# Kernel tuning notes

Hardware: AMD Instinct MI355X
Metric: run time of the kernel (lower is better)

## Reference

```python
import jax, jax.numpy as jnp
import numpy as np

CONFIDENCE = 0.1
EPS = 1e-3  # keras BatchNormalization default epsilon
B, H, W, C = 4, 64, 64, 256


def setup_inputs() -> dict:
    key = jax.random.key(0)
    ks = jax.random.split(key, 6)
    return {
        "x": jax.random.normal(ks[0], (B, H, W, C), jnp.float32),
        "ca_gamma": jnp.ones((C,), jnp.float32),
        "ca_beta": jnp.zeros((C,), jnp.float32),
        "ca_mean": jnp.zeros((C,), jnp.float32),
        "ca_var": jnp.ones((C,), jnp.float32),
        "wq": jax.random.normal(ks[1], (C, C), jnp.float32) * 0.05,
        "wk": jax.random.normal(ks[2], (C, C), jnp.float32) * 0.05,
        "wv": jax.random.normal(ks[3], (C, C), jnp.float32) * 0.05,
        "wp": jax.random.normal(ks[4], (C, C), jnp.float32) * 0.05,
        "bn_gamma": jnp.ones((C,), jnp.float32),
        "bn_beta": jnp.zeros((C,), jnp.float32),
        "bn_mean": jnp.zeros((C,), jnp.float32),
        "bn_var": jnp.ones((C,), jnp.float32),
        "w_qkv": jax.random.normal(ks[5], (C, 3), jnp.float32) * 0.05,
    }


def _bn(x, g, b, m, v):
    # keras BatchNormalization, inference mode
    return (x - m) * jax.lax.rsqrt(v + EPS) * g + b


def reference(x, ca_gamma, ca_beta, ca_mean, ca_var, wq, wk, wv, wp,
              bn_gamma, bn_beta, bn_mean, bn_var, w_qkv):
    b, h, w, c = x.shape
    # ---- ChannelAttention (TRACER Channel_Tracer; dropout = identity at inference) ----
    gap = x.mean(axis=(1, 2))                         # [B, C] global average pool
    gn = _bn(gap, ca_gamma, ca_beta, ca_mean, ca_var)  # [B, C]
    q = gn @ wq                                        # 1x1 conv on 1x1 map == matmul
    k = gn @ wk
    v = gn @ wv
    logits = q[:, :, None] * k[:, None, :]             # [B, C, C], head_dim = 1
    score = jax.nn.softmax(logits, axis=-1)
    att = jnp.einsum('bij,bj->bi', score, v)           # [B, C]
    cmask = jax.nn.sigmoid(att @ wp)                   # [B, C] channel mask (alpha)
    ca_out = x * cmask[:, None, None, :] + x           # residual channel re-weighting
    # ---- UnionAttention spatial part ----
    co = _bn(ca_out, bn_gamma, bn_beta, bn_mean, bn_var)
    thr = jnp.percentile(cmask, CONFIDENCE * 100.0, axis=-1,
                         keepdims=True, method='linear')  # [B, 1]
    pmask = jnp.where(cmask > thr, cmask, 0.0)          # percentile masking
    co = co * pmask[:, None, None, :]
    qkv = jnp.einsum('bhwc,cf->bhwf', co, w_qkv)        # [B, H, W, 3] fused q/k/v 1x1 conv
    n = h * w
    qs = qkv[..., 0].reshape(b, n)                      # [B, N], head_dim = 1
    ks_ = qkv[..., 1].reshape(b, n)
    vs = qkv[..., 2].reshape(b, n)
    sl = qs[:, :, None] * ks_[:, None, :]               # [B, N, N] scores (outer product)
    sw = jax.nn.softmax(sl, axis=-1)
    sa = jnp.einsum('bij,bj->bi', sw, vs)               # [B, N]
    return qkv[..., 2:3] + sa.reshape(b, h, w, 1)       # v + attention, [B, H, W, 1]
```

## Files before the change

kernel.cpp:

```cpp
#include <hip/hip_runtime.h>

#define EPS 1e-3f

#define OFF_PGAP   0
#define OFF_A      65536
#define OFF_BIAS   66560
#define OFF_QS     66576
#define OFF_KS     82960
#define OFF_VS     99344
#define OFF_PART   115728

__global__ __launch_bounds__(256) void k_gap(const float* __restrict__ x,
                                             float* __restrict__ pgap) {
    int blk = blockIdx.x;
    int t = threadIdx.x;
    const float* xp = x + (size_t)blk * (64 * 256) + t;
    float s = 0.f;
    #pragma unroll 16
    for (int p = 0; p < 64; ++p) s += xp[(size_t)p * 256];
    pgap[blk * 256 + t] = s;
}

__global__ __launch_bounds__(512) void k_mid(
    const float* __restrict__ pgap,
    const float* __restrict__ cag, const float* __restrict__ cab,
    const float* __restrict__ cam, const float* __restrict__ cav,
    const float* __restrict__ wq, const float* __restrict__ wk,
    const float* __restrict__ wv, const float* __restrict__ wp,
    const float* __restrict__ bng, const float* __restrict__ bnb,
    const float* __restrict__ bnm, const float* __restrict__ bnv,
    const float* __restrict__ wqkv,
    float* __restrict__ Aout, float* __restrict__ biasOut)
{
    __shared__ float gn[256];
    __shared__ float sq[256], sk[256], sv[256], att[256], cm[256], Bc[256];
    __shared__ float red[6144];
    __shared__ float swqkv[768];
    __shared__ float t25, t26, thr;

    int b = blockIdx.x;
    int t = threadIdx.x;
    int cg = t & 63;
    int rg = t >> 6;
    int c4 = cg * 4;

    if (t < 384) {
        swqkv[t] = wqkv[t];
        if (t < 384) swqkv[t + 384] = wqkv[t + 384];
    }

    {
        const float* pg = pgap + (size_t)(b * 64 + rg * 8) * 256 + c4;
        float4 s = make_float4(0.f, 0.f, 0.f, 0.f);
        #pragma unroll
        for (int u = 0; u < 8; ++u) {
            float4 v = *(const float4*)(pg + (size_t)u * 256);
            s.x += v.x; s.y += v.y; s.z += v.z; s.w += v.w;
        }
        *(float4*)(red + rg * 256 + c4) = s;
    }
    __syncthreads();
    if (t < 256) {
        float g = 0.f;
        #pragma unroll
        for (int r = 0; r < 8; ++r) g += red[r * 256 + t];
        g *= (1.0f / 4096.0f);
        float sc = cag[t] * rsqrtf(cav[t] + EPS);
        gn[t] = g * sc + (cab[t] - cam[t] * sc);
    }
    __syncthreads();

    {
        int rbase = rg * 32;
        float4 aq = make_float4(0.f, 0.f, 0.f, 0.f);
        float4 ak = aq, av = aq;
        const float* wqp = wq + (size_t)rbase * 256 + c4;
        const float* wkp = wk + (size_t)rbase * 256 + c4;
        const float* wvp = wv + (size_t)rbase * 256 + c4;
        #pragma unroll 8
        for (int i = 0; i < 32; ++i) {
            float g = gn[rbase + i];
            float4 w = *(const float4*)(wqp + (size_t)i * 256);
            aq.x = fmaf(g, w.x, aq.x); aq.y = fmaf(g, w.y, aq.y);
            aq.z = fmaf(g, w.z, aq.z); aq.w = fmaf(g, w.w, aq.w);
        }
        #pragma unroll 8
        for (int i = 0; i < 32; ++i) {
            float g = gn[rbase + i];
            float4 w = *(const float4*)(wkp + (size_t)i * 256);
            ak.x = fmaf(g, w.x, ak.x); ak.y = fmaf(g, w.y, ak.y);
            ak.z = fmaf(g, w.z, ak.z); ak.w = fmaf(g, w.w, ak.w);
        }
        #pragma unroll 8
        for (int i = 0; i < 32; ++i) {
            float g = gn[rbase + i];
            float4 w = *(const float4*)(wvp + (size_t)i * 256);
            av.x = fmaf(g, w.x, av.x); av.y = fmaf(g, w.y, av.y);
            av.z = fmaf(g, w.z, av.z); av.w = fmaf(g, w.w, av.w);
        }
        *(float4*)(red + (0 * 8 + rg) * 256 + c4) = aq;
        *(float4*)(red + (1 * 8 + rg) * 256 + c4) = ak;
        *(float4*)(red + (2 * 8 + rg) * 256 + c4) = av;
    }
    __syncthreads();
    {
        int m = t >> 8, c = t & 255;
        float s = 0.f;
        #pragma unroll
        for (int r = 0; r < 8; ++r) s += red[(m * 8 + r) * 256 + c];
        if (m == 0) sq[c] = s; else sk[c] = s;
        if (t < 256) {
            float s2 = 0.f;
            #pragma unroll
            for (int r = 0; r < 8; ++r) s2 += red[(2 * 8 + r) * 256 + t];
            sv[t] = s2;
        }
    }
    __syncthreads();

    {
        int h = t >> 8, c = t & 255;
        float a = sq[c];
        int jb = h * 128;
        float mx = -1e30f;
        #pragma unroll 8
        for (int j = 0; j < 128; ++j) mx = fmaxf(mx, a * sk[jb + j]);
        float den = 0.f, num = 0.f;
        #pragma unroll 4
        for (int j = 0; j < 128; ++j) {
            float e = __expf(a * sk[jb + j] - mx);
            den += e; num = fmaf(e, sv[jb + j], num);
        }
        red[h * 256 + c] = mx;
        red[512 + h * 256 + c] = den;
        red[1024 + h * 256 + c] = num;
    }
    __syncthreads();
    if (t < 256) {
        float m0 = red[t], m1 = red[256 + t];
        float M = fmaxf(m0, m1);
        float s0 = __expf(m0 - M), s1 = __expf(m1 - M);
        float den = red[512 + t] * s0 + red[768 + t] * s1;
        float num = red[1024 + t] * s0 + red[1280 + t] * s1;
        att[t] = num / den;
    }
    __syncthreads();

    {
        int rbase = rg * 32;
        float4 ac = make_float4(0.f, 0.f, 0.f, 0.f);
        const float* wpp = wp + (size_t)rbase * 256 + c4;
        #pragma unroll 8
        for (int i = 0; i < 32; ++i) {
            float g = att[rbase + i];
            float4 w = *(const float4*)(wpp + (size_t)i * 256);
            ac.x = fmaf(g, w.x, ac.x); ac.y = fmaf(g, w.y, ac.y);
            ac.z = fmaf(g, w.z, ac.z); ac.w = fmaf(g, w.w, ac.w);
        }
        *(float4*)(red + rg * 256 + c4) = ac;
    }
    __syncthreads();
    if (t < 256) {
        float ac = 0.f;
        #pragma unroll
        for (int r = 0; r < 8; ++r) ac += red[r * 256 + t];
        cm[t] = 1.0f / (1.0f + __expf(-ac));
    }
    __syncthreads();

    if (t < 256) {
        float my = cm[t];
        int rank = 0;
        for (int j = 0; j < 256; ++j) {
            float o = cm[j];
            rank += (o < my) ? 1 : ((o == my && j < t) ? 1 : 0);
        }
        if (rank == 25) t25 = my;
        if (rank == 26) t26 = my;
    }
    __syncthreads();
    if (t == 0) thr = t25 + 0.5f * (t26 - t25);
    __syncthreads();

    if (t < 256) {
        float s2 = bng[t] * rsqrtf(bnv[t] + EPS);
        float o2 = bnb[t] - bnm[t] * s2;
        float cc = cm[t];
        float pm = (cc > thr) ? cc : 0.f;
        Aout[b * 256 + t] = (1.f + cc) * s2 * pm;
        Bc[t] = o2 * pm;
    }
    __syncthreads();
    if (t < 3) {
        float s3 = 0.f;
        for (int ch = 0; ch < 256; ++ch) s3 = fmaf(Bc[ch], swqkv[ch * 3 + t], s3);
        biasOut[b * 3 + t] = s3;
    }
}

__global__ __launch_bounds__(256) void k_qkv(
    const float* __restrict__ x, const float* __restrict__ A,
    const float* __restrict__ wqkv, const float* __restrict__ bias,
    float* __restrict__ qs, float* __restrict__ ks, float* __restrict__ vs)
{
    int lane = threadIdx.x & 63;
    int wid = (blockIdx.x * 256 + threadIdx.x) >> 6;
    float4 wA = *(const float4*)(wqkv + 12 * lane);
    float4 wB = *(const float4*)(wqkv + 12 * lane + 4);
    float4 wC = *(const float4*)(wqkv + 12 * lane + 8);
    float w00 = wA.x, w01 = wA.y, w02 = wA.z;
    float w10 = wA.w, w11 = wB.x, w12 = wB.y;
    float w20 = wB.z, w21 = wB.w, w22 = wC.x;
    float w30 = wC.y, w31 = wC.z, w32 = wC.w;
    #pragma unroll
    for (int b = 0; b < 4; ++b) {
        int pix = b * 4096 + wid;
        float4 xv = *(const float4*)(x + (size_t)pix * 256 + 4 * lane);
        float4 A4 = *(const float4*)(A + b * 256 + 4 * lane);
        float t0 = xv.x * A4.x, t1 = xv.y * A4.y;
        float t2 = xv.z * A4.z, t3 = xv.w * A4.w;
        float q = t0 * w00 + t1 * w10 + t2 * w20 + t3 * w30;
        float k = t0 * w01 + t1 * w11 + t2 * w21 + t3 * w31;
        float v = t0 * w02 + t1 * w12 + t2 * w22 + t3 * w32;
        #pragma unroll
        for (int m = 1; m < 64; m <<= 1) {
            q += __shfl_xor(q, m, 64);
            k += __shfl_xor(k, m, 64);
            v += __shfl_xor(v, m, 64);
        }
        if (lane == 0) {
            qs[pix] = q + bias[b * 3 + 0];
            ks[pix] = k + bias[b * 3 + 1];
            vs[pix] = v + bias[b * 3 + 2];
        }
    }
}

__global__ __launch_bounds__(256) void k_attn(
    const float* __restrict__ qs, const float* __restrict__ ks, const float* __restrict__ vs,
    float* __restrict__ part)
{
    __shared__ float4 skv4[256];
    __shared__ float wmx[4], wmn[4];
    int blk = blockIdx.x;
    int b = blk >> 7, rem = blk & 127;
    int ic = rem >> 3, jc = rem & 7;
    int t = threadIdx.x;
    int base = b * 4096, jb = jc * 512;
    float2 kp = ((const float2*)(ks + base + jb))[t];
    float2 vp = ((const float2*)(vs + base + jb))[t];
    skv4[t] = make_float4(kp.x, vp.x, kp.y, vp.y);
    float mx = fmaxf(kp.x, kp.y);
    float mn = fminf(kp.x, kp.y);
    #pragma unroll
    for (int m2 = 1; m2 < 64; m2 <<= 1) {
        mx = fmaxf(mx, __shfl_xor(mx, m2, 64));
        mn = fminf(mn, __shfl_xor(mn, m2, 64));
    }
    if ((t & 63) == 0) { wmx[t >> 6] = mx; wmn[t >> 6] = mn; }
    __syncthreads();
    mx = fmaxf(fmaxf(wmx[0], wmx[1]), fmaxf(wmx[2], wmx[3]));
    mn = fminf(fminf(wmn[0], wmn[1]), fminf(wmn[2], wmn[3]));

    int i = ic * 256 + t;
    float a = qs[base + i];
    float m = (a >= 0.f) ? a * mx : a * mn;
    float den0 = 0.f, num0 = 0.f, den1 = 0.f, num1 = 0.f;
    #pragma unroll 4
    for (int j2 = 0; j2 < 256; ++j2) {
        float4 kv = skv4[j2];
        float e0 = __expf(a * kv.x - m);
        float e1 = __expf(a * kv.z - m);
        den0 += e0; num0 = fmaf(e0, kv.y, num0);
        den1 += e1; num1 = fmaf(e1, kv.w, num1);
    }
    ((float4*)part)[(size_t)(base + i) * 8 + jc] =
        make_float4(den0 + den1, num0 + num1, m, 0.f);
}

__global__ __launch_bounds__(256) void k_out(
    const float* __restrict__ part, const float* __restrict__ vs,
    float* __restrict__ out)
{
    int t = blockIdx.x * 256 + threadIdx.x;
    const float4* p4 = (const float4*)part + (size_t)t * 8;
    float4 p[8];
    #pragma unroll
    for (int c = 0; c < 8; ++c) p[c] = p4[c];
    float M = p[0].z;
    #pragma unroll
    for (int c = 1; c < 8; ++c) M = fmaxf(M, p[c].z);
    float den = 0.f, num = 0.f;
    #pragma unroll
    for (int c = 0; c < 8; ++c) {
        float sc = __expf(p[c].z - M);
        den = fmaf(p[c].x, sc, den);
        num = fmaf(p[c].y, sc, num);
    }
    out[t] = vs[t] + num / den;
}

extern "C" void kernel_launch(void* const* d_in, const int* in_sizes, int n_in,
                              void* d_out, int out_size, void* d_ws, size_t ws_size,
                              hipStream_t stream) {
    const float* x    = (const float*)d_in[0];
    const float* cag  = (const float*)d_in[1];
    const float* cab  = (const float*)d_in[2];
    const float* cam  = (const float*)d_in[3];
    const float* cav  = (const float*)d_in[4];
    const float* wq   = (const float*)d_in[5];
    const float* wk   = (const float*)d_in[6];
    const float* wv   = (const float*)d_in[7];
    const float* wp   = (const float*)d_in[8];
    const float* bng  = (const float*)d_in[9];
    const float* bnb  = (const float*)d_in[10];
    const float* bnm  = (const float*)d_in[11];
    const float* bnv  = (const float*)d_in[12];
    const float* wqkv = (const float*)d_in[13];

    float* ws   = (float*)d_ws;
    float* pgap = ws + OFF_PGAP;
    float* A    = ws + OFF_A;
    float* bias = ws + OFF_BIAS;
    float* qs   = ws + OFF_QS;
    float* ks   = ws + OFF_KS;
    float* vs   = ws + OFF_VS;
    float* part = ws + OFF_PART;

    k_gap<<<dim3(256), dim3(256), 0, stream>>>(x, pgap);
    k_mid<<<dim3(4), dim3(512), 0, stream>>>(pgap, cag, cab, cam, cav, wq, wk, wv, wp,
                                             bng, bnb, bnm, bnv, wqkv, A, bias);
    k_qkv<<<dim3(1024), dim3(256), 0, stream>>>(x, A, wqkv, bias, qs, ks, vs);
    k_attn<<<dim3(512), dim3(256), 0, stream>>>(qs, ks, vs, part);
    k_out<<<dim3(64), dim3(256), 0, stream>>>(part, vs, (float*)d_out);
}
```

Before: 141.5 us.

## Fuse spatial attention partial-softmax and combine kernels into one block-level reduction

The separate attention and combine kernels become one kernel. Each 512-thread block now loads all 4096 keys and values of a batch into shared memory and splits them across 8 wavefronts for 64 query rows, then reduces the partial sums in shared memory and writes the output directly. This drops the partial-results round trip through global memory and one kernel launch. In exchange each block stages the full key/value set and there are fewer, larger blocks (256 instead of 512). All partials share the same row max, so no rescaling is needed.

```diff
diff --git a/kernel.cpp b/kernel.cpp
--- a/kernel.cpp
+++ b/kernel.cpp
@@ -8,7 +8,6 @@
 #define OFF_QS     66576
 #define OFF_KS     82960
 #define OFF_VS     99344
-#define OFF_PART   115728
 
 __global__ __launch_bounds__(256) void k_gap(const float* __restrict__ x,
                                              float* __restrict__ pgap) {
@@ -46,7 +45,7 @@
 
     if (t < 384) {
         swqkv[t] = wqkv[t];
-        if (t < 384) swqkv[t + 384] = wqkv[t + 384];
+        swqkv[t + 384] = wqkv[t + 384];
     }
 
     {
@@ -236,68 +235,66 @@
     }
 }
 
-__global__ __launch_bounds__(256) void k_attn(
+__global__ __launch_bounds__(512) void k_attn2(
     const float* __restrict__ qs, const float* __restrict__ ks, const float* __restrict__ vs,
-    float* __restrict__ part)
+    float* __restrict__ out)
 {
-    __shared__ float4 skv4[256];
-    __shared__ float wmx[4], wmn[4];
+    __shared__ float4 skv[2048];
+    __shared__ float pden[8][64], pnum[8][64];
+    __shared__ float rmax[8], rmin[8];
     int blk = blockIdx.x;
-    int b = blk >> 7, rem = blk & 127;
-    int ic = rem >> 3, jc = rem & 7;
+    int b = blk >> 6, ic = blk & 63;
     int t = threadIdx.x;
-    int base = b * 4096, jb = jc * 512;
-    float2 kp = ((const float2*)(ks + base + jb))[t];
-    float2 vp = ((const float2*)(vs + base + jb))[t];
-    skv4[t] = make_float4(kp.x, vp.x, kp.y, vp.y);
-    float mx = fmaxf(kp.x, kp.y);
-    float mn = fminf(kp.x, kp.y);
+    int lane = t & 63, sub = t >> 6;
+    int base = b * 4096;
+
+    const float4* k4 = (const float4*)(ks + base);
+    const float4* v4 = (const float4*)(vs + base);
+    float kmx = -1e30f, kmn = 1e30f;
+    #pragma unroll
+    for (int u = 0; u < 2; ++u) {
+        int i = t + u * 512;
+        float4 kk = k4[i], vv = v4[i];
+        skv[i * 2]     = make_float4(kk.x, vv.x, kk.y, vv.y);
+        skv[i * 2 + 1] = make_float4(kk.z, vv.z, kk.w, vv.w);
+        kmx = fmaxf(kmx, fmaxf(fmaxf(kk.x, kk.y), fmaxf(kk.z, kk.w)));
+        kmn = fminf(kmn, fminf(fminf(kk.x, kk.y), fminf(kk.z, kk.w)));
+    }
     #pragma unroll
     for (int m2 = 1; m2 < 64; m2 <<= 1) {
-        mx = fmaxf(mx, __shfl_xor(mx, m2, 64));
-        mn = fminf(mn, __shfl_xor(mn, m2, 64));
-    }
-    if ((t & 63) == 0) { wmx[t >> 6] = mx; wmn[t >> 6] = mn; }
-    __syncthreads();
-    mx = fmaxf(fmaxf(wmx[0], wmx[1]), fmaxf(wmx[2], wmx[3]));
-    mn = fminf(fminf(wmn[0], wmn[1]), fminf(wmn[2], wmn[3]));
-
-    int i = ic * 256 + t;
-    float a = qs[base + i];
+        kmx = fmaxf(kmx, __shfl_xor(kmx, m2, 64));
+        kmn = fminf(kmn, __shfl_xor(kmn, m2, 64));
+    }
+    if (lane == 0) { rmax[sub] = kmx; rmin[sub] = kmn; }
+    __syncthreads();
+    float mx = rmax[0], mn = rmin[0];
+    #pragma unroll
+    for (int s = 1; s < 8; ++s) { mx = fmaxf(mx, rmax[s]); mn = fminf(mn, rmin[s]); }
+
+    int row = ic * 64 + lane;
+    float a = qs[base + row];
     float m = (a >= 0.f) ? a * mx : a * mn;
     float den0 = 0.f, num0 = 0.f, den1 = 0.f, num1 = 0.f;
+    const float4* sp = skv + sub * 256;
     #pragma unroll 4
-    for (int j2 = 0; j2 < 256; ++j2) {
-        float4 kv = skv4[j2];
-        float e0 = __expf(a * kv.x - m);
-        float e1 = __expf(a * kv.z - m);
+    for (int j = 0; j < 256; ++j) {
+        float4 kv = sp[j];
+        float e0 = __expf(fmaf(a, kv.x, -m));
+        float e1 = __expf(fmaf(a, kv.z, -m));
         den0 += e0; num0 = fmaf(e0, kv.y, num0);
         den1 += e1; num1 = fmaf(e1, kv.w, num1);
     }
-    ((float4*)part)[(size_t)(base + i) * 8 + jc] =
-        make_float4(den0 + den1, num0 + num1, m, 0.f);
-}
-
-__global__ __launch_bounds__(256) void k_out(
-    const float* __restrict__ part, const float* __restrict__ vs,
-    float* __restrict__ out)
-{
-    int t = blockIdx.x * 256 + threadIdx.x;
-    const float4* p4 = (const float4*)part + (size_t)t * 8;
-    float4 p[8];
-    #pragma unroll
-    for (int c = 0; c < 8; ++c) p[c] = p4[c];
-    float M = p[0].z;
-    #pragma unroll
-    for (int c = 1; c < 8; ++c) M = fmaxf(M, p[c].z);
-    float den = 0.f, num = 0.f;
-    #pragma unroll
-    for (int c = 0; c < 8; ++c) {
-        float sc = __expf(p[c].z - M);
-        den = fmaf(p[c].x, sc, den);
-        num = fmaf(p[c].y, sc, num);
-    }
-    out[t] = vs[t] + num / den;
+    pden[sub][lane] = den0 + den1;
+    pnum[sub][lane] = num0 + num1;
+    __syncthreads();
+    if (t < 64) {
+        float den = 0.f, num = 0.f;
+        #pragma unroll
+        for (int s = 0; s < 8; ++s) { den += pden[s][t]; num += pnum[s][t]; }
+        int r = ic * 64 + t;
+        float vrow = (r & 1) ? skv[r >> 1].w : skv[r >> 1].y;
+        out[base + r] = vrow + num / den;
+    }
 }
 
 extern "C" void kernel_launch(void* const* d_in, const int* in_sizes, int n_in,
@@ -325,12 +322,10 @@
     float* qs   = ws + OFF_QS;
     float* ks   = ws + OFF_KS;
     float* vs   = ws + OFF_VS;
-    float* part = ws + OFF_PART;
 
     k_gap<<<dim3(256), dim3(256), 0, stream>>>(x, pgap);
     k_mid<<<dim3(4), dim3(512), 0, stream>>>(pgap, cag, cab, cam, cav, wq, wk, wv, wp,
                                              bng, bnb, bnm, bnv, wqkv, A, bias);
     k_qkv<<<dim3(1024), dim3(256), 0, stream>>>(x, A, wqkv, bias, qs, ks, vs);
-    k_attn<<<dim3(512), dim3(256), 0, stream>>>(qs, ks, vs, part);
-    k_out<<<dim3(64), dim3(256), 0, stream>>>(part, vs, (float*)d_out);
-}
+    k_attn2<<<dim3(256), dim3(512), 0, stream>>>(qs, ks, vs, (float*)d_out);
+}
```

Result: no change. 139.3 us (-1.6%).
